# Performance work log

Hardware: AMD Instinct MI355X
Metric: run time of the kernel (lower is better)

The kernel has to match this reference:

```python
import jax, jax.numpy as jnp
import numpy as np
import math

N_HEADS = 12
HEAD_DIM = 64
D_MODEL = 768
BATCH = 2
SEQ = 2048
GRID = 46  # num_patches_per_side


def _rope_1d(x, pos, dim):
    # x: (B,S,H,dim), pos: (S,) int -> rotary embedding along last dim
    inv_freq = 1.0 / (10000.0 ** (jnp.arange(0, dim, 2, dtype=jnp.float32) / dim))  # (dim/2,)
    ang = pos.astype(jnp.float32)[:, None] * inv_freq  # (S, dim/2)
    cos = jnp.concatenate([jnp.cos(ang), jnp.cos(ang)], axis=-1)[None, :, None, :]
    sin = jnp.concatenate([jnp.sin(ang), jnp.sin(ang)], axis=-1)[None, :, None, :]
    x1, x2 = jnp.split(x, 2, axis=-1)
    rot = jnp.concatenate([-x2, x1], axis=-1)
    return x * cos.astype(x.dtype) + rot * sin.astype(x.dtype)


def _rope_2d(x, row_ids, col_ids):
    # 2D RoPE: first half of head_dim rotated by row position, second half by column position
    half = x.shape[-1] // 2
    xr = _rope_1d(x[..., :half], row_ids, half)
    xc = _rope_1d(x[..., half:], col_ids, half)
    return jnp.concatenate([xr, xc], axis=-1)


def setup_inputs() -> dict:
    key = jax.random.key(0)
    ks = jax.random.split(key, 7)
    scale = 1.0 / math.sqrt(D_MODEL)
    return {
        "x": jax.random.normal(ks[0], (BATCH, SEQ, D_MODEL), dtype=jnp.float32),
        "row_ids": jax.random.randint(ks[1], (SEQ,), 0, GRID),
        "col_ids": jax.random.randint(ks[2], (SEQ,), 0, GRID),
        "Wq": jax.random.normal(ks[3], (D_MODEL, D_MODEL), dtype=jnp.float32) * scale,
        "Wk": jax.random.normal(ks[4], (D_MODEL, D_MODEL), dtype=jnp.float32) * scale,
        "Wv": jax.random.normal(ks[5], (D_MODEL, D_MODEL), dtype=jnp.float32) * scale,
        "Wo": jax.random.normal(ks[6], (D_MODEL, D_MODEL), dtype=jnp.float32) * scale,
    }


def reference(x, row_ids, col_ids, Wq, Wk, Wv, Wo):
    B, S, _ = x.shape
    # projections (nn.Linear: y = x @ W.T)
    q = (x @ Wq.T).reshape(B, S, N_HEADS, HEAD_DIM)
    k = (x @ Wk.T).reshape(B, S, N_HEADS, HEAD_DIM)
    v = (x @ Wv.T).reshape(B, S, N_HEADS, HEAD_DIM)
    q = _rope_2d(q, row_ids, col_ids)
    k = _rope_2d(k, row_ids, col_ids)
    # (B,H,S,D)
    q = q.transpose(0, 2, 1, 3)
    k = k.transpose(0, 2, 1, 3)
    v = v.transpose(0, 2, 1, 3)
    scale = 1.0 / math.sqrt(HEAD_DIM)
    scores = jnp.einsum('bhqd,bhkd->bhqk', q, k) * scale  # (B,H,S,S)
    causal = jnp.triu(jnp.ones((S, S), dtype=bool), k=1)
    scores = jnp.where(causal, -jnp.inf, scores)
    attn = jax.nn.softmax(scores, axis=-1)
    out = jnp.einsum('bhqk,bhkd->bhqd', attn, v)
    out = out.transpose(0, 2, 1, 3).reshape(B, S, D_MODEL)
    return out @ Wo.T
```

## Files before the change

kernel.cpp:

```cpp
#include <hip/hip_runtime.h>
#include <stdint.h>
#include <stddef.h>

#define DEV __device__ __forceinline__

typedef unsigned short u16;
typedef __attribute__((ext_vector_type(8))) __bf16 bf16x8;
typedef __attribute__((ext_vector_type(4))) float f32x4;
typedef __attribute__((ext_vector_type(8))) unsigned short u16x8;
typedef __attribute__((ext_vector_type(4))) unsigned short u16x4;

DEV u16 f2bf(float f) {
  uint32_t u = __builtin_bit_cast(uint32_t, f);
  u += 0x7fffu + ((u >> 16) & 1u);
  return (u16)(u >> 16);
}
DEV float bf2f(u16 h) {
  uint32_t u = ((uint32_t)h) << 16;
  return __builtin_bit_cast(float, u);
}
DEV f32x4 mfma16(bf16x8 a, bf16x8 b, f32x4 c) {
  return __builtin_amdgcn_mfma_f32_16x16x32_bf16(a, b, c, 0, 0, 0);
}
DEV void ld_lds16(const void* g, void* l) {
  __builtin_amdgcn_global_load_lds((const __attribute__((address_space(1))) void*)g,
                                   (__attribute__((address_space(3))) void*)l, 16, 0, 0);
}

__global__ __launch_bounds__(256) void k_cvt_all(const float* __restrict__ x,
                                                 const float* __restrict__ wq,
                                                 const float* __restrict__ wk,
                                                 const float* __restrict__ wv,
                                                 const float* __restrict__ wo,
                                                 u16* __restrict__ dx,
                                                 u16* __restrict__ dqkv,
                                                 u16* __restrict__ dwo) {
  const int bid = blockIdx.x;
  const float* src;
  u16* dst;
  int off;
  if (bid < 3072) {
    src = x; dst = dx; off = bid;
  } else {
    const int t = bid - 3072;
    const int w = t / 576;
    off = t - w * 576;
    src = (w == 0) ? wq : (w == 1) ? wk : (w == 2) ? wv : wo;
    dst = (w < 3) ? (dqkv + (size_t)w * 589824) : dwo;
  }
  const int i = (off * 256 + threadIdx.x) * 4;
  const float4 f = *(const float4*)(src + i);
  u16x4 o;
  o.x = f2bf(f.x); o.y = f2bf(f.y); o.z = f2bf(f.z); o.w = f2bf(f.w);
  *(u16x4*)(dst + i) = o;
}

template <bool OUT_F32>
__global__ __launch_bounds__(256, 4) void k_gemm64(const u16* __restrict__ A,
                                                   const u16* __restrict__ B,
                                                   void* __restrict__ Cv,
                                                   int N, int K) {
  __shared__ __align__(16) u16 sA[64 * 64];
  __shared__ __align__(16) u16 sB[128 * 64];
  const int tid = threadIdx.x;
  const int lane = tid & 63;
  const int wid = tid >> 6;
  const int col16 = lane & 15, quad = lane >> 4;
  const int rowBase = blockIdx.y * 64;
  const int colBase = blockIdx.x * 128;
  const int seg_r = lane >> 3;
  const int seg_c = lane & 7;

  f32x4 zero; zero[0] = zero[1] = zero[2] = zero[3] = 0.0f;
  f32x4 acc[4][2];
#pragma unroll
  for (int i = 0; i < 4; ++i) { acc[i][0] = zero; acc[i][1] = zero; }

  for (int k0 = 0; k0 < K; k0 += 64) {
#pragma unroll
    for (int c = 0; c < 2; ++c) {
      const int seg = wid * 2 + c;
      ld_lds16(A + (size_t)(rowBase + seg * 8 + seg_r) * K + k0 + seg_c * 8, sA + seg * 512);
    }
#pragma unroll
    for (int c = 0; c < 4; ++c) {
      const int seg = wid * 4 + c;
      ld_lds16(B + (size_t)(colBase + seg * 8 + seg_r) * K + k0 + seg_c * 8, sB + seg * 512);
    }
    __syncthreads();
#pragma unroll
    for (int kk = 0; kk < 2; ++kk) {
      bf16x8 af[4], bfr[2];
#pragma unroll
      for (int t = 0; t < 4; ++t)
        af[t] = *(const bf16x8*)(sA + (t * 16 + col16) * 64 + kk * 32 + quad * 8);
#pragma unroll
      for (int t = 0; t < 2; ++t)
        bfr[t] = *(const bf16x8*)(sB + (wid * 32 + t * 16 + col16) * 64 + kk * 32 + quad * 8);
#pragma unroll
      for (int tm = 0; tm < 4; ++tm)
#pragma unroll
        for (int tn = 0; tn < 2; ++tn)
          acc[tm][tn] = mfma16(af[tm], bfr[tn], acc[tm][tn]);
    }
    __syncthreads();
  }

#pragma unroll
  for (int tm = 0; tm < 4; ++tm)
#pragma unroll
    for (int tn = 0; tn < 2; ++tn)
#pragma unroll
      for (int r = 0; r < 4; ++r) {
        const int row = rowBase + tm * 16 + quad * 4 + r;
        const int col = colBase + wid * 32 + tn * 16 + col16;
        const float v = acc[tm][tn][r];
        if (OUT_F32) ((float*)Cv)[(size_t)row * N + col] = v;
        else         ((u16*)Cv)[(size_t)row * N + col] = f2bf(v);
      }
}

__global__ __launch_bounds__(256) void k_rope_vtrans(const u16* __restrict__ QKV,
                                                     const int* __restrict__ row_ids,
                                                     const int* __restrict__ col_ids,
                                                     u16* __restrict__ Qh,
                                                     u16* __restrict__ Kh,
                                                     u16* __restrict__ Vt) {
  __shared__ __align__(16) u16 tile[64][72];
  if (blockIdx.x < 6144) {
    const int t = blockIdx.x * 256 + threadIdx.x;
    const int p = t & 31;
    const int rest = t >> 5;
    const int h = rest % 12;
    const int bs = rest / 12;
    const int s = bs & 2047;
    const int b = bs >> 11;
    const int f = p & 15;
    const int hs = p >> 4;
    const int pos = hs ? col_ids[s] : row_ids[s];
    const float ang = (float)pos * expf(-(float)f * 0.5756462732485114f);
    float sn, cs;
    sincosf(ang, &sn, &cs);
    const int d1 = hs * 32 + f;
    const int d2 = d1 + 16;
    const size_t ibase = (size_t)bs * 2304 + h * 64;
    const size_t obase = (((size_t)b * 12 + h) * 2048 + s) * 64;
    {
      const float x1 = bf2f(QKV[ibase + d1]);
      const float x2 = bf2f(QKV[ibase + d2]);
      Qh[obase + d1] = f2bf(x1 * cs - x2 * sn);
      Qh[obase + d2] = f2bf(x2 * cs + x1 * sn);
    }
    {
      const float x1 = bf2f(QKV[ibase + 768 + d1]);
      const float x2 = bf2f(QKV[ibase + 768 + d2]);
      Kh[obase + d1] = f2bf(x1 * cs - x2 * sn);
      Kh[obase + d2] = f2bf(x2 * cs + x1 * sn);
    }
  } else {
    const int vb = blockIdx.x - 6144;
    const int s0 = (vb & 31) * 64;
    const int bh = vb >> 5;
    const int b = bh / 12, h = bh % 12;
    const int tid = threadIdx.x;
    const int rl = tid >> 2;
    const int cb = (tid & 3) * 16;
    const u16* src = QKV + ((size_t)b * 2048 + s0 + rl) * 2304 + 1536 + h * 64 + cb;
    const u16x8 v0 = *(const u16x8*)src;
    const u16x8 v1 = *(const u16x8*)(src + 8);
    *(u16x8*)&tile[rl][cb] = v0;
    *(u16x8*)&tile[rl][cb + 8] = v1;
    __syncthreads();
    u16x8 o0, o1;
#pragma unroll
    for (int j = 0; j < 8; ++j) {
      o0[j] = tile[cb + j][rl];
      o1[j] = tile[cb + 8 + j][rl];
    }
    u16* dst = Vt + ((size_t)bh * 64 + rl) * 2048 + s0 + cb;
    *(u16x8*)dst = o0;
    *(u16x8*)(dst + 8) = o1;
  }
}

__global__ __launch_bounds__(256, 3) void k_attn(const u16* __restrict__ Qh,
                                                 const u16* __restrict__ Kh,
                                                 const u16* __restrict__ Vt,
                                                 u16* __restrict__ O) {
  __shared__ __align__(16) u16 sK[2][64 * 64];
  __shared__ __align__(16) u16 sV[2][64 * 64];
  __shared__ __align__(16) u16 sP[4][16 * 72];
  const int tid = threadIdx.x;
  const int lane = tid & 63;
  const int wid = tid >> 6;
  const int col16 = lane & 15;
  const int quad = lane >> 4;
  const int fIdx = blockIdx.x;
  const int b3 = fIdx & 7;
  const int r = fIdx >> 3;
  const int g = r >> 5;
  const int qt = 31 - (r & 31);
  const int bh = b3 + 8 * g;
  const int b = bh / 12, h = bh % 12;
  const int qw = qt * 64 + wid * 16;
  const int nkt = qt + 1;

  const u16* Qb = Qh + (size_t)bh * (2048 * 64);
  const u16* Kb = Kh + (size_t)bh * (2048 * 64);
  const u16* Vb = Vt + (size_t)bh * (64 * 2048);

  const bf16x8 bQ0 = *(const bf16x8*)(Qb + (size_t)(qw + col16) * 64 + quad * 8);
  const bf16x8 bQ1 = *(const bf16x8*)(Qb + (size_t)(qw + col16) * 64 + 32 + quad * 8);

  f32x4 zero; zero[0] = zero[1] = zero[2] = zero[3] = 0.0f;
  f32x4 o[4];
#pragma unroll
  for (int i = 0; i < 4; ++i) o[i] = zero;
  float m_r = -1e30f, l_r = 0.0f;

  u16* sPw = &sP[wid][0];

  auto stage = [&](int buf, int kt) {
#pragma unroll
    for (int c = 0; c < 2; ++c) {
      const int kc = wid * 2 + c;
      ld_lds16(Kb + (size_t)kt * 64 + kc * 512 + lane * 8, &sK[buf][kc * 512]);
      ld_lds16(Vb + (size_t)(kc * 8 + (lane >> 3)) * 2048 + kt + (lane & 7) * 8,
               &sV[buf][kc * 512]);
    }
  };

  stage(0, 0);
  __syncthreads();

  for (int ki = 0; ki < nkt; ++ki) {
    const int buf = ki & 1;
    const int kt = ki * 64;
    if (ki + 1 < nkt) stage(buf ^ 1, kt + 64);
    bf16x8 ka0[4], ka1[4], va0[4], va1[4];
#pragma unroll
    for (int tn = 0; tn < 4; ++tn) {
      const int base = (tn * 16 + col16) * 64 + quad * 8;
      ka0[tn] = *(const bf16x8*)&sK[buf][base];
      ka1[tn] = *(const bf16x8*)&sK[buf][base + 32];
      va0[tn] = *(const bf16x8*)&sV[buf][base];
      va1[tn] = *(const bf16x8*)&sV[buf][base + 32];
    }
    f32x4 sc[4];
#pragma unroll
    for (int tn = 0; tn < 4; ++tn)
      sc[tn] = mfma16(ka1[tn], bQ1, mfma16(ka0[tn], bQ0, zero));
    const bool diag = (ki == nkt - 1);
#pragma unroll
    for (int tn = 0; tn < 4; ++tn)
#pragma unroll
      for (int rr = 0; rr < 4; ++rr) {
        float v = sc[tn][rr] * 0.125f;
        if (diag && (kt + tn * 16 + quad * 4 + rr > qw + col16)) v = -1e30f;
        sc[tn][rr] = v;
      }
    float vm = sc[0][0];
#pragma unroll
    for (int tn = 0; tn < 4; ++tn)
#pragma unroll
      for (int rr = 0; rr < 4; ++rr) vm = fmaxf(vm, sc[tn][rr]);
    vm = fmaxf(vm, __shfl_xor(vm, 16, 64));
    vm = fmaxf(vm, __shfl_xor(vm, 32, 64));
    const float mn = fmaxf(m_r, vm);
    const float alpha = __expf(m_r - mn);
    m_r = mn;
    float rs = 0.0f;
#pragma unroll
    for (int tn = 0; tn < 4; ++tn)
#pragma unroll
      for (int h2 = 0; h2 < 2; ++h2) {
        const float p0 = __expf(sc[tn][2 * h2] - mn);
        const float p1 = __expf(sc[tn][2 * h2 + 1] - mn);
        rs += p0 + p1;
        const uint32_t w = (uint32_t)f2bf(p0) | ((uint32_t)f2bf(p1) << 16);
        ((uint32_t*)sPw)[col16 * 36 + tn * 8 + quad * 2 + h2] = w;
      }
    rs += __shfl_xor(rs, 16, 64);
    rs += __shfl_xor(rs, 32, 64);
    l_r = l_r * alpha + rs;
#pragma unroll
    for (int t = 0; t < 4; ++t)
#pragma unroll
      for (int rr = 0; rr < 4; ++rr) o[t][rr] *= alpha;
    asm volatile("s_waitcnt lgkmcnt(0)" ::: "memory");
    const bf16x8 bP0 = *(const bf16x8*)(sPw + col16 * 72 + quad * 8);
    const bf16x8 bP1 = *(const bf16x8*)(sPw + col16 * 72 + 32 + quad * 8);
#pragma unroll
    for (int tn = 0; tn < 4; ++tn)
      o[tn] = mfma16(va1[tn], bP1, mfma16(va0[tn], bP0, o[tn]));
    __syncthreads();
  }

  const float invl = 1.0f / l_r;
  const size_t row = (size_t)b * 2048 + qw + col16;
#pragma unroll
  for (int tn = 0; tn < 4; ++tn)
#pragma unroll
    for (int h2 = 0; h2 < 2; ++h2) {
      const float v0 = o[tn][2 * h2] * invl;
      const float v1 = o[tn][2 * h2 + 1] * invl;
      const uint32_t w = (uint32_t)f2bf(v0) | ((uint32_t)f2bf(v1) << 16);
      const int col = h * 64 + tn * 16 + quad * 4 + 2 * h2;
      *(uint32_t*)(O + row * 768 + col) = w;
    }
}

extern "C" void kernel_launch(void* const* d_in, const int* in_sizes, int n_in,
                              void* d_out, int out_size, void* d_ws, size_t ws_size,
                              hipStream_t stream) {
  const float* x       = (const float*)d_in[0];
  const int*   row_ids = (const int*)d_in[1];
  const int*   col_ids = (const int*)d_in[2];
  const float* Wq      = (const float*)d_in[3];
  const float* Wk      = (const float*)d_in[4];
  const float* Wv      = (const float*)d_in[5];
  const float* Wo      = (const float*)d_in[6];
  float* out = (float*)d_out;

  uint8_t* w8 = (uint8_t*)d_ws;
  u16* x_bf = (u16*)(w8 + 0);
  u16* wqkv = (u16*)(w8 + 6291456);
  u16* wo   = (u16*)(w8 + 9830400);
  u16* qkv  = (u16*)(w8 + 11010048);
  u16* qh   = (u16*)(w8 + 29884416);
  u16* kh   = (u16*)(w8 + 36175872);
  u16* vt   = (u16*)(w8 + 42467328);
  u16* obuf = (u16*)(w8 + 48758784);

  k_cvt_all<<<5376, 256, 0, stream>>>(x, Wq, Wk, Wv, Wo, x_bf, wqkv, wo);
  k_gemm64<false><<<dim3(18, 64), 256, 0, stream>>>(x_bf, wqkv, (void*)qkv, 2304, 768);
  k_rope_vtrans<<<6912, 256, 0, stream>>>(qkv, row_ids, col_ids, qh, kh, vt);
  k_attn<<<768, 256, 0, stream>>>(qh, kh, vt, obuf);
  k_gemm64<true><<<dim3(6, 64), 256, 0, stream>>>(obuf, wo, (void*)out, 768, 768);
}
```

Before: 207.0 us.

## Rework attention to two-wave blocks with 32 query rows each; add 64x64 output GEMM

The attention kernel now uses 128 threads per block, and each wave handles two 16-row query groups. Each K/V fragment read from LDS is therefore reused across twice as many query rows. K/V staging changes from direct global-to-LDS loads to register prefetch into padded LDS tiles, which avoids bank conflicts, and causal masking is now skipped per group where it cannot apply. A new 64x64-tile output projection GEMM replaces the generic kernel to launch more blocks for the small N=768 case. The costs are higher register pressure in attention and fewer waves per block to hide latency.

```diff
diff --git a/kernel.cpp b/kernel.cpp
--- a/kernel.cpp
+++ b/kernel.cpp
@@ -117,6 +117,71 @@
         const float v = acc[tm][tn][r];
         if (OUT_F32) ((float*)Cv)[(size_t)row * N + col] = v;
         else         ((u16*)Cv)[(size_t)row * N + col] = f2bf(v);
+      }
+}
+
+__global__ __launch_bounds__(256, 3) void k_gemm_o(const u16* __restrict__ A,
+                                                   const u16* __restrict__ B,
+                                                   float* __restrict__ C,
+                                                   int N, int K) {
+  __shared__ __align__(16) u16 sA[64 * 72];
+  __shared__ __align__(16) u16 sB[64 * 72];
+  const int tid = threadIdx.x;
+  const int lane = tid & 63;
+  const int wid = tid >> 6;
+  const int col16 = lane & 15, quad = lane >> 4;
+  const int wm = wid & 1, wn = wid >> 1;
+  const int rowBase = blockIdx.y * 64;
+  const int colBase = blockIdx.x * 64;
+  const int sr = tid >> 3;
+  const int sc8 = (tid & 7) * 8;
+
+  f32x4 zero; zero[0] = zero[1] = zero[2] = zero[3] = 0.0f;
+  f32x4 acc[2][2];
+  acc[0][0] = zero; acc[0][1] = zero; acc[1][0] = zero; acc[1][1] = zero;
+
+  u16x8 ar[2], br[2];
+  auto gload = [&](int k0) {
+    ar[0] = *(const u16x8*)(A + (size_t)(rowBase + sr) * K + k0 + sc8);
+    ar[1] = *(const u16x8*)(A + (size_t)(rowBase + 32 + sr) * K + k0 + sc8);
+    br[0] = *(const u16x8*)(B + (size_t)(colBase + sr) * K + k0 + sc8);
+    br[1] = *(const u16x8*)(B + (size_t)(colBase + 32 + sr) * K + k0 + sc8);
+  };
+
+  gload(0);
+  for (int k0 = 0; k0 < K; k0 += 64) {
+    __syncthreads();
+    *(u16x8*)&sA[sr * 72 + sc8] = ar[0];
+    *(u16x8*)&sA[(32 + sr) * 72 + sc8] = ar[1];
+    *(u16x8*)&sB[sr * 72 + sc8] = br[0];
+    *(u16x8*)&sB[(32 + sr) * 72 + sc8] = br[1];
+    if (k0 + 64 < K) gload(k0 + 64);
+    __syncthreads();
+#pragma unroll
+    for (int kk = 0; kk < 2; ++kk) {
+      bf16x8 af[2], bfr[2];
+#pragma unroll
+      for (int t = 0; t < 2; ++t) {
+        af[t]  = *(const bf16x8*)&sA[(wm * 32 + t * 16 + col16) * 72 + kk * 32 + quad * 8];
+        bfr[t] = *(const bf16x8*)&sB[(wn * 32 + t * 16 + col16) * 72 + kk * 32 + quad * 8];
+      }
+#pragma unroll
+      for (int tm = 0; tm < 2; ++tm)
+#pragma unroll
+        for (int tn = 0; tn < 2; ++tn)
+          acc[tm][tn] = mfma16(af[tm], bfr[tn], acc[tm][tn]);
+    }
+  }
+
+#pragma unroll
+  for (int tm = 0; tm < 2; ++tm)
+#pragma unroll
+    for (int tn = 0; tn < 2; ++tn)
+#pragma unroll
+      for (int r = 0; r < 4; ++r) {
+        const int row = rowBase + wm * 32 + tm * 16 + quad * 4 + r;
+        const int col = colBase + wn * 32 + tn * 16 + col16;
+        C[(size_t)row * N + col] = acc[tm][tn][r];
       }
 }
 
@@ -183,13 +248,13 @@
   }
 }
 
-__global__ __launch_bounds__(256, 3) void k_attn(const u16* __restrict__ Qh,
+__global__ __launch_bounds__(128, 2) void k_attn(const u16* __restrict__ Qh,
                                                  const u16* __restrict__ Kh,
                                                  const u16* __restrict__ Vt,
                                                  u16* __restrict__ O) {
-  __shared__ __align__(16) u16 sK[2][64 * 64];
-  __shared__ __align__(16) u16 sV[2][64 * 64];
-  __shared__ __align__(16) u16 sP[4][16 * 72];
+  __shared__ __align__(16) u16 sK[2][64 * 72];
+  __shared__ __align__(16) u16 sV[2][64 * 72];
+  __shared__ __align__(16) u16 sP[2][32 * 72];
   const int tid = threadIdx.x;
   const int lane = tid & 63;
   const int wid = tid >> 6;
@@ -197,117 +262,163 @@
   const int quad = lane >> 4;
   const int fIdx = blockIdx.x;
   const int b3 = fIdx & 7;
-  const int r = fIdx >> 3;
-  const int g = r >> 5;
-  const int qt = 31 - (r & 31);
-  const int bh = b3 + 8 * g;
+  const int r_ = fIdx >> 3;
+  const int g_ = r_ >> 5;
+  const int qt = 31 - (r_ & 31);
+  const int bh = b3 + 8 * g_;
   const int b = bh / 12, h = bh % 12;
-  const int qw = qt * 64 + wid * 16;
+  const int qw = qt * 64 + wid * 32;
   const int nkt = qt + 1;
 
   const u16* Qb = Qh + (size_t)bh * (2048 * 64);
   const u16* Kb = Kh + (size_t)bh * (2048 * 64);
   const u16* Vb = Vt + (size_t)bh * (64 * 2048);
 
-  const bf16x8 bQ0 = *(const bf16x8*)(Qb + (size_t)(qw + col16) * 64 + quad * 8);
-  const bf16x8 bQ1 = *(const bf16x8*)(Qb + (size_t)(qw + col16) * 64 + 32 + quad * 8);
+  const int sr = tid >> 3;
+  const int sc8 = (tid & 7) * 8;
+
+  bf16x8 bQ[2][2];
+#pragma unroll
+  for (int g = 0; g < 2; ++g) {
+    const u16* qp = Qb + (size_t)(qw + g * 16 + col16) * 64 + quad * 8;
+    bQ[g][0] = *(const bf16x8*)qp;
+    bQ[g][1] = *(const bf16x8*)(qp + 32);
+  }
 
   f32x4 zero; zero[0] = zero[1] = zero[2] = zero[3] = 0.0f;
-  f32x4 o[4];
-#pragma unroll
-  for (int i = 0; i < 4; ++i) o[i] = zero;
-  float m_r = -1e30f, l_r = 0.0f;
+  f32x4 o[2][4];
+#pragma unroll
+  for (int g = 0; g < 2; ++g)
+#pragma unroll
+    for (int i = 0; i < 4; ++i) o[g][i] = zero;
+  float m_r[2] = {-1e30f, -1e30f}, l_r[2] = {0.0f, 0.0f};
 
   u16* sPw = &sP[wid][0];
 
-  auto stage = [&](int buf, int kt) {
-#pragma unroll
-    for (int c = 0; c < 2; ++c) {
-      const int kc = wid * 2 + c;
-      ld_lds16(Kb + (size_t)kt * 64 + kc * 512 + lane * 8, &sK[buf][kc * 512]);
-      ld_lds16(Vb + (size_t)(kc * 8 + (lane >> 3)) * 2048 + kt + (lane & 7) * 8,
-               &sV[buf][kc * 512]);
+  u16x8 kr[4], vr[4];
+  auto gload = [&](int kt) {
+#pragma unroll
+    for (int i = 0; i < 4; ++i) {
+      const int row = sr + i * 16;
+      kr[i] = *(const u16x8*)(Kb + (size_t)(kt + row) * 64 + sc8);
+      vr[i] = *(const u16x8*)(Vb + (size_t)row * 2048 + kt + sc8);
     }
   };
-
-  stage(0, 0);
+  auto lwrite = [&](int buf) {
+#pragma unroll
+    for (int i = 0; i < 4; ++i) {
+      const int row = sr + i * 16;
+      *(u16x8*)&sK[buf][row * 72 + sc8] = kr[i];
+      *(u16x8*)&sV[buf][row * 72 + sc8] = vr[i];
+    }
+  };
+
+  gload(0);
+  lwrite(0);
+  if (nkt > 1) gload(64);
   __syncthreads();
 
   for (int ki = 0; ki < nkt; ++ki) {
     const int buf = ki & 1;
     const int kt = ki * 64;
-    if (ki + 1 < nkt) stage(buf ^ 1, kt + 64);
-    bf16x8 ka0[4], ka1[4], va0[4], va1[4];
+    if (ki + 1 < nkt) {
+      lwrite(buf ^ 1);
+      if (ki + 2 < nkt) gload(kt + 128);
+    }
+    bf16x8 ka0[4], ka1[4];
 #pragma unroll
     for (int tn = 0; tn < 4; ++tn) {
-      const int base = (tn * 16 + col16) * 64 + quad * 8;
+      const int base = (tn * 16 + col16) * 72 + quad * 8;
       ka0[tn] = *(const bf16x8*)&sK[buf][base];
       ka1[tn] = *(const bf16x8*)&sK[buf][base + 32];
+    }
+    f32x4 sc[2][4];
+#pragma unroll
+    for (int tn = 0; tn < 4; ++tn) {
+      sc[0][tn] = mfma16(ka1[tn], bQ[0][1], mfma16(ka0[tn], bQ[0][0], zero));
+      sc[1][tn] = mfma16(ka1[tn], bQ[1][1], mfma16(ka0[tn], bQ[1][0], zero));
+    }
+    bf16x8 va0[4], va1[4];
+#pragma unroll
+    for (int tn = 0; tn < 4; ++tn) {
+      const int base = (tn * 16 + col16) * 72 + quad * 8;
       va0[tn] = *(const bf16x8*)&sV[buf][base];
       va1[tn] = *(const bf16x8*)&sV[buf][base + 32];
     }
-    f32x4 sc[4];
+#pragma unroll
+    for (int g = 0; g < 2; ++g) {
+      const int qrow = qw + g * 16 + col16;
+      if (kt + 63 > qw + g * 16) {
+#pragma unroll
+        for (int tn = 0; tn < 4; ++tn)
+#pragma unroll
+          for (int rr = 0; rr < 4; ++rr) {
+            float v = sc[g][tn][rr] * 0.125f;
+            if (kt + tn * 16 + quad * 4 + rr > qrow) v = -1e30f;
+            sc[g][tn][rr] = v;
+          }
+      } else {
+#pragma unroll
+        for (int tn = 0; tn < 4; ++tn)
+#pragma unroll
+          for (int rr = 0; rr < 4; ++rr) sc[g][tn][rr] *= 0.125f;
+      }
+      float vm = sc[g][0][0];
+#pragma unroll
+      for (int tn = 0; tn < 4; ++tn)
+#pragma unroll
+        for (int rr = 0; rr < 4; ++rr) vm = fmaxf(vm, sc[g][tn][rr]);
+      vm = fmaxf(vm, __shfl_xor(vm, 16, 64));
+      vm = fmaxf(vm, __shfl_xor(vm, 32, 64));
+      const float mn = fmaxf(m_r[g], vm);
+      const float alpha = __expf(m_r[g] - mn);
+      m_r[g] = mn;
+      float rs = 0.0f;
+#pragma unroll
+      for (int tn = 0; tn < 4; ++tn)
+#pragma unroll
+        for (int h2 = 0; h2 < 2; ++h2) {
+          const float p0 = __expf(sc[g][tn][2 * h2] - mn);
+          const float p1 = __expf(sc[g][tn][2 * h2 + 1] - mn);
+          rs += p0 + p1;
+          const uint32_t w = (uint32_t)f2bf(p0) | ((uint32_t)f2bf(p1) << 16);
+          ((uint32_t*)sPw)[(g * 16 + col16) * 36 + tn * 8 + quad * 2 + h2] = w;
+        }
+      rs += __shfl_xor(rs, 16, 64);
+      rs += __shfl_xor(rs, 32, 64);
+      l_r[g] = l_r[g] * alpha + rs;
+#pragma unroll
+      for (int t = 0; t < 4; ++t)
+#pragma unroll
+        for (int rr = 0; rr < 4; ++rr) o[g][t][rr] *= alpha;
+    }
+    asm volatile("s_waitcnt lgkmcnt(0)" ::: "memory");
+#pragma unroll
+    for (int g = 0; g < 2; ++g) {
+      const bf16x8 bP0 = *(const bf16x8*)(sPw + (g * 16 + col16) * 72 + quad * 8);
+      const bf16x8 bP1 = *(const bf16x8*)(sPw + (g * 16 + col16) * 72 + 32 + quad * 8);
+#pragma unroll
+      for (int tn = 0; tn < 4; ++tn)
+        o[g][tn] = mfma16(va1[tn], bP1, mfma16(va0[tn], bP0, o[g][tn]));
+    }
+    __syncthreads();
+  }
+
+#pragma unroll
+  for (int g = 0; g < 2; ++g) {
+    const float invl = 1.0f / l_r[g];
+    const size_t row = (size_t)b * 2048 + qw + g * 16 + col16;
 #pragma unroll
     for (int tn = 0; tn < 4; ++tn)
-      sc[tn] = mfma16(ka1[tn], bQ1, mfma16(ka0[tn], bQ0, zero));
-    const bool diag = (ki == nkt - 1);
-#pragma unroll
-    for (int tn = 0; tn < 4; ++tn)
-#pragma unroll
-      for (int rr = 0; rr < 4; ++rr) {
-        float v = sc[tn][rr] * 0.125f;
-        if (diag && (kt + tn * 16 + quad * 4 + rr > qw + col16)) v = -1e30f;
-        sc[tn][rr] = v;
+#pragma unroll
+      for (int h2 = 0; h2 < 2; ++h2) {
+        const float v0 = o[g][tn][2 * h2] * invl;
+        const float v1 = o[g][tn][2 * h2 + 1] * invl;
+        const uint32_t w = (uint32_t)f2bf(v0) | ((uint32_t)f2bf(v1) << 16);
+        const int col = h * 64 + tn * 16 + quad * 4 + 2 * h2;
+        *(uint32_t*)(O + row * 768 + col) = w;
       }
-    float vm = sc[0][0];
-#pragma unroll
-    for (int tn = 0; tn < 4; ++tn)
-#pragma unroll
-      for (int rr = 0; rr < 4; ++rr) vm = fmaxf(vm, sc[tn][rr]);
-    vm = fmaxf(vm, __shfl_xor(vm, 16, 64));
-    vm = fmaxf(vm, __shfl_xor(vm, 32, 64));
-    const float mn = fmaxf(m_r, vm);
-    const float alpha = __expf(m_r - mn);
-    m_r = mn;
-    float rs = 0.0f;
-#pragma unroll
-    for (int tn = 0; tn < 4; ++tn)
-#pragma unroll
-      for (int h2 = 0; h2 < 2; ++h2) {
-        const float p0 = __expf(sc[tn][2 * h2] - mn);
-        const float p1 = __expf(sc[tn][2 * h2 + 1] - mn);
-        rs += p0 + p1;
-        const uint32_t w = (uint32_t)f2bf(p0) | ((uint32_t)f2bf(p1) << 16);
-        ((uint32_t*)sPw)[col16 * 36 + tn * 8 + quad * 2 + h2] = w;
-      }
-    rs += __shfl_xor(rs, 16, 64);
-    rs += __shfl_xor(rs, 32, 64);
-    l_r = l_r * alpha + rs;
-#pragma unroll
-    for (int t = 0; t < 4; ++t)
-#pragma unroll
-      for (int rr = 0; rr < 4; ++rr) o[t][rr] *= alpha;
-    asm volatile("s_waitcnt lgkmcnt(0)" ::: "memory");
-    const bf16x8 bP0 = *(const bf16x8*)(sPw + col16 * 72 + quad * 8);
-    const bf16x8 bP1 = *(const bf16x8*)(sPw + col16 * 72 + 32 + quad * 8);
-#pragma unroll
-    for (int tn = 0; tn < 4; ++tn)
-      o[tn] = mfma16(va1[tn], bP1, mfma16(va0[tn], bP0, o[tn]));
-    __syncthreads();
-  }
-
-  const float invl = 1.0f / l_r;
-  const size_t row = (size_t)b * 2048 + qw + col16;
-#pragma unroll
-  for (int tn = 0; tn < 4; ++tn)
-#pragma unroll
-    for (int h2 = 0; h2 < 2; ++h2) {
-      const float v0 = o[tn][2 * h2] * invl;
-      const float v1 = o[tn][2 * h2 + 1] * invl;
-      const uint32_t w = (uint32_t)f2bf(v0) | ((uint32_t)f2bf(v1) << 16);
-      const int col = h * 64 + tn * 16 + quad * 4 + 2 * h2;
-      *(uint32_t*)(O + row * 768 + col) = w;
-    }
+  }
 }
 
 extern "C" void kernel_launch(void* const* d_in, const int* in_sizes, int n_in,
@@ -335,6 +446,6 @@
   k_cvt_all<<<5376, 256, 0, stream>>>(x, Wq, Wk, Wv, Wo, x_bf, wqkv, wo);
   k_gemm64<false><<<dim3(18, 64), 256, 0, stream>>>(x_bf, wqkv, (void*)qkv, 2304, 768);
   k_rope_vtrans<<<6912, 256, 0, stream>>>(qkv, row_ids, col_ids, qh, kh, vt);
-  k_attn<<<768, 256, 0, stream>>>(qh, kh, vt, obuf);
-  k_gemm64<true><<<dim3(6, 64), 256, 0, stream>>>(obuf, wo, (void*)out, 768, 768);
-}
+  k_attn<<<768, 128, 0, stream>>>(qh, kh, vt, obuf);
+  k_gemm_o<<<dim3(12, 64), 256, 0, stream>>>(obuf, wo, out, 768, 768);
+}
```

Result: no change. 205.9 us (-0.6%).
